# Kernel optimization log

Hardware: AMD Instinct MI355X
Metric: run time of the kernel (lower is better)

## Reference

```python
import jax, jax.numpy as jnp
import numpy as np

B, IN_LEN, N_VARS, PRED_LEN, E, TOPK = 64, 1024, 512, 1024, 8, 2


def setup_inputs() -> dict:
    key = jax.random.key(0)
    k1, k2, k3, k4 = jax.random.split(key, 4)
    x = jax.random.normal(k1, (B, IN_LEN, N_VARS), dtype=jnp.float32)
    # Gating: nn.Linear(seq_len, n_experts, bias=False) -> store as [seq, E] (x @ gate_W)
    gate_W = jax.random.normal(k2, (IN_LEN, E), dtype=jnp.float32) / np.sqrt(IN_LEN).astype(np.float32)
    # experts: nn.Linear(seq_len, pred_len) each -> stacked [E, seq, pred], bias [E, pred]
    expert_W = jax.random.normal(k3, (E, IN_LEN, PRED_LEN), dtype=jnp.float32) / np.sqrt(IN_LEN).astype(np.float32)
    expert_b = jax.random.normal(k4, (E, PRED_LEN), dtype=jnp.float32) * 0.01
    return {"x": x, "gate_W": gate_W, "expert_W": expert_W, "expert_b": expert_b}


def reference(x, gate_W, expert_W, expert_b):
    # x: [B, in_len, n_vars] -> tokens are (batch, variable) pairs of length in_len
    xt = jnp.transpose(x, (0, 2, 1))                      # [B, N, S]
    gate = jax.nn.softmax(xt @ gate_W, axis=-1)           # [B, N, E] (softmaxed logits, as in torch code)
    weights, sel = jax.lax.top_k(gate, TOPK)              # [B, N, K]
    # combine[b,n,e] = sum_k weights[b,n,k] * 1[sel[b,n,k]==e]  (scatter of top-k weights)
    combine = jnp.sum(weights[..., None] * jax.nn.one_hot(sel, E, dtype=x.dtype), axis=2)  # [B, N, E]
    # masked dense combine: identical math to gather->Linear->weighted scatter-add
    out = jnp.zeros((xt.shape[0], xt.shape[1], PRED_LEN), dtype=x.dtype)
    for e in range(E):  # small fixed expert loop
        y_e = xt @ expert_W[e] + expert_b[e]              # [B, N, P]
        out = out + combine[:, :, e:e + 1] * y_e
    out = jnp.transpose(out, (0, 2, 1))                   # [B, pred_len, n_vars]
    gate_mean = jnp.mean(gate, axis=0)                    # [N, E] == gate_logits.mean(dim=0)
    return (out, gate_mean)
```

## Files before the change

kernel.cpp:

```cpp
#include <hip/hip_runtime.h>
#include <cstddef>

typedef __bf16 bf16x8 __attribute__((ext_vector_type(8)));
typedef float  f32x4  __attribute__((ext_vector_type(4)));
typedef unsigned short u16x8 __attribute__((ext_vector_type(8)));

#define GLOBAL_AS __attribute__((address_space(1)))
#define LDS_AS    __attribute__((address_space(3)))

__device__ __forceinline__ void gload_lds16(const void* g, void* l) {
    __builtin_amdgcn_global_load_lds((const GLOBAL_AS unsigned int*)g,
                                     (LDS_AS unsigned int*)l, 16, 0, 0);
}

__device__ __forceinline__ unsigned short f2bf(float f) {
    union { float f; unsigned int u; } v; v.f = f;
    unsigned int r = v.u + 0x7FFFu + ((v.u >> 16) & 1u);
    return (unsigned short)(r >> 16);
}
__device__ __forceinline__ float bf2f(unsigned short h) {
    union { unsigned int u; float f; } v; v.u = ((unsigned int)h) << 16;
    return v.f;
}

__global__ __launch_bounds__(256) void transpose_cast_kernel(
    const float* __restrict__ src, unsigned short* __restrict__ dst,
    int R, int C)
{
    const int bat = blockIdx.z;
    src += (size_t)bat * R * C;
    dst += (size_t)bat * R * C;
    const int r0 = blockIdx.y * 64, c0 = blockIdx.x * 64;
    __shared__ float t[64][65];
    const int tid = threadIdx.x;
    const int rr = tid >> 4;
    const int cc = (tid & 15) * 4;

    #pragma unroll
    for (int p = 0; p < 4; p++) {
        int r = p * 16 + rr;
        const float4 v = *reinterpret_cast<const float4*>(&src[(size_t)(r0 + r) * C + c0 + cc]);
        t[r][cc + 0] = v.x; t[r][cc + 1] = v.y; t[r][cc + 2] = v.z; t[r][cc + 3] = v.w;
    }
    __syncthreads();
    #pragma unroll
    for (int p = 0; p < 4; p++) {
        int c = p * 16 + rr;
        ushort4 o;
        o.x = f2bf(t[cc + 0][c]); o.y = f2bf(t[cc + 1][c]);
        o.z = f2bf(t[cc + 2][c]); o.w = f2bf(t[cc + 3][c]);
        *reinterpret_cast<ushort4*>(&dst[(size_t)(c0 + c) * R + r0 + cc]) = o;
    }
}

__global__ __launch_bounds__(256) void transpose_x_gate_kernel(
    const float* __restrict__ src, const float* __restrict__ gW,
    unsigned short* __restrict__ dst, float* __restrict__ plog)
{
    const int bat = blockIdx.z;
    const int R = 1024, C = 512;
    const float* srcb = src + (size_t)bat * R * C;
    unsigned short* dstb = dst + (size_t)bat * R * C;
    const int r0 = blockIdx.y * 64, c0 = blockIdx.x * 64;
    __shared__ float t[64][65];
    __shared__ float gWs[64][8];
    __shared__ float pacc[4][64][9];
    const int tid = threadIdx.x;
    const int rr = tid >> 4;
    const int cc = (tid & 15) * 4;

    if (tid < 128) {
        reinterpret_cast<float4*>(&gWs[0][0])[tid] =
            reinterpret_cast<const float4*>(gW + (size_t)r0 * 8)[tid];
    }
    #pragma unroll
    for (int p = 0; p < 4; p++) {
        int r = p * 16 + rr;
        const float4 v = *reinterpret_cast<const float4*>(&srcb[(size_t)(r0 + r) * C + c0 + cc]);
        t[r][cc + 0] = v.x; t[r][cc + 1] = v.y; t[r][cc + 2] = v.z; t[r][cc + 3] = v.w;
    }
    __syncthreads();
    #pragma unroll
    for (int p = 0; p < 4; p++) {
        int c = p * 16 + rr;
        ushort4 o;
        o.x = f2bf(t[cc + 0][c]); o.y = f2bf(t[cc + 1][c]);
        o.z = f2bf(t[cc + 2][c]); o.w = f2bf(t[cc + 3][c]);
        *reinterpret_cast<ushort4*>(&dstb[(size_t)(c0 + c) * R + r0 + cc]) = o;
    }

    {
        const int nl = tid & 63;
        const int sc = tid >> 6;
        float a[8];
        #pragma unroll
        for (int e = 0; e < 8; e++) a[e] = 0.f;
        for (int s = sc * 16; s < sc * 16 + 16; s++) {
            float xv = t[s][nl];
            #pragma unroll
            for (int e = 0; e < 8; e++) a[e] = fmaf(xv, gWs[s][e], a[e]);
        }
        #pragma unroll
        for (int e = 0; e < 8; e++) pacc[sc][nl][e] = a[e];
        __syncthreads();
        if (tid < 64) {
            const size_t base = (((size_t)bat * 16 + blockIdx.y) * 512 + c0 + tid) * 8;
            #pragma unroll
            for (int e = 0; e < 8; e++) {
                float v = ((pacc[0][tid][e] + pacc[1][tid][e]) + pacc[2][tid][e]) + pacc[3][tid][e];
                plog[base + e] = v;
            }
        }
    }
}

__global__ __launch_bounds__(256) void gate_stage2_kernel(
    const float* __restrict__ plog,
    float* __restrict__ gate, int* __restrict__ e01,
    float* __restrict__ w0a, float* __restrict__ w1a,
    int* __restrict__ hist)
{
    __shared__ int h[16];
    const int tid = threadIdx.x;
    if (tid < 16) h[tid] = 0;
    __syncthreads();

    const int t = blockIdx.x * 256 + tid;
    const int b = t >> 9;
    const int n = t & 511;

    float acc[8];
    #pragma unroll
    for (int e = 0; e < 8; e++) acc[e] = 0.f;
    for (int y = 0; y < 16; y++) {
        const float* pp = plog + (((size_t)b * 16 + y) * 512 + n) * 8;
        const float4 lo = *reinterpret_cast<const float4*>(pp);
        const float4 hi = *reinterpret_cast<const float4*>(pp + 4);
        acc[0] += lo.x; acc[1] += lo.y; acc[2] += lo.z; acc[3] += lo.w;
        acc[4] += hi.x; acc[5] += hi.y; acc[6] += hi.z; acc[7] += hi.w;
    }
    float m = acc[0];
    #pragma unroll
    for (int e = 1; e < 8; e++) m = fmaxf(m, acc[e]);
    float p[8], s = 0.f;
    #pragma unroll
    for (int e = 0; e < 8; e++) { p[e] = __expf(acc[e] - m); s += p[e]; }
    float inv = 1.f / s;
    #pragma unroll
    for (int e = 0; e < 8; e++) p[e] *= inv;

    int e0 = 0;
    #pragma unroll
    for (int e = 1; e < 8; e++) if (p[e] > p[e0]) e0 = e;
    int e1 = -1;
    #pragma unroll
    for (int e = 0; e < 8; e++) {
        if (e == e0) continue;
        if (e1 < 0 || p[e] > p[e1]) e1 = e;
    }

    const size_t base = (size_t)t * 8;
    #pragma unroll
    for (int e = 0; e < 8; e++) gate[base + e] = p[e];
    e01[t] = e0 | (e1 << 8);
    w0a[t] = p[e0];
    w1a[t] = p[e1];

    atomicAdd(&h[e0], 1);
    atomicAdd(&h[8 + e1], 1);
    __syncthreads();
    if (tid < 16) hist[blockIdx.x * 16 + tid] = h[tid];
}

__global__ __launch_bounds__(256) void gate_mean_kernel(
    const float* __restrict__ gate, float* __restrict__ out)
{
    const int idx = blockIdx.x * 256 + threadIdx.x;
    float s = 0.f;
    #pragma unroll 8
    for (int b = 0; b < 64; b++) s += gate[(size_t)b * 4096 + idx];
    out[idx] = s * (1.f / 64.f);
}

__global__ __launch_bounds__(256) void scan_kernel(
    const int* __restrict__ hist, int* __restrict__ chunk_off,
    int* __restrict__ meta)
{
    __shared__ int cnt_s[16];
    const int tid = threadIdx.x;
    if (tid < 16) {
        int run = 0;
        for (int c = 0; c < 128; c++) {
            chunk_off[c * 16 + tid] = run;
            run += hist[c * 16 + tid];
        }
        cnt_s[tid] = run;
        meta[16 + tid] = run;
    }
    __syncthreads();
    __shared__ int base_s[16];
    if (tid == 0) {
        int run = 0, trun = 0;
        meta[32] = 0;
        for (int g = 0; g < 16; g++) {
            base_s[g] = run;
            meta[g] = run;
            run += cnt_s[g];
            trun += (cnt_s[g] + 255) >> 8;
            meta[33 + g] = trun;
        }
    }
    __syncthreads();
    for (int i = tid; i < 2048; i += 256)
        chunk_off[i] += base_s[i & 15];
}

__global__ __launch_bounds__(256) void fill_kernel(
    const int* __restrict__ e01, const int* __restrict__ chunk_off,
    int* __restrict__ perm, int* __restrict__ posA, int* __restrict__ posB)
{
    __shared__ int wh[4][16];
    const int tid = threadIdx.x;
    const int wv = tid >> 6, lane = tid & 63;
    const int chunk = blockIdx.x;
    const int t = chunk * 256 + tid;
    const int ev = e01[t];
    const int e0 = ev & 255, e1 = ev >> 8;

    const unsigned long long ltmask = (lane == 63) ? 0x7FFFFFFFFFFFFFFFull
                                                   : ((1ull << lane) - 1ull);
    unsigned long long m0sel = 0, m1sel = 0;
    #pragma unroll
    for (int e = 0; e < 8; e++) {
        unsigned long long b0 = __ballot(e0 == e);
        unsigned long long b1 = __ballot(e1 == e);
        if (e0 == e) m0sel = b0;
        if (e1 == e) m1sel = b1;
        if (lane == 0) {
            wh[wv][e]     = __popcll(b0);
            wh[wv][8 + e] = __popcll(b1);
        }
    }
    const int r0l = __popcll(m0sel & ltmask);
    const int r1l = __popcll(m1sel & ltmask);
    __syncthreads();

    int off0 = 0, off1 = 0;
    for (int w = 0; w < wv; w++) { off0 += wh[w][e0]; off1 += wh[w][8 + e1]; }

    const int p0 = chunk_off[chunk * 16 + e0] + off0 + r0l;
    const int p1 = chunk_off[chunk * 16 + 8 + e1] + off1 + r1l;
    perm[p0] = t; perm[p1] = t;
    posA[t] = p0; posB[t] = p1;
}

__global__ __launch_bounds__(512, 2) void grouped_gemm_kernel(
    const unsigned short* __restrict__ Wt,
    const unsigned short* __restrict__ xt,
    const int* __restrict__ perm,
    const int* __restrict__ meta,
    const float* __restrict__ expert_b,
    unsigned short* __restrict__ tmp)
{
    const int d    = blockIdx.x;
    const int xcd  = d & 7;
    const int jj   = d >> 3;
    const int tile = xcd * 34 + (jj >> 2);
    const int p0   = (jj & 3) * 256;

    int g = -1;
    #pragma unroll
    for (int gg = 0; gg < 16; gg++) {
        if (tile >= meta[32 + gg] && tile < meta[33 + gg]) g = gg;
    }
    if (g < 0) return;
    const int lt = tile - meta[32 + g];
    const int e = g & 7;
    const int cnt_local = meta[16 + g] - lt * 256;
    const int pbase = meta[g] + lt * 256;

    __shared__ unsigned short As[2][256 * 64];
    __shared__ unsigned short Bs[2][256 * 64];

    const int tid  = threadIdx.x;
    const int wid  = tid >> 6, lane = tid & 63;
    const int wr = wid >> 2, wc = wid & 3;
    const int q = lane >> 4, r16 = lane & 15;

    const int srow   = tid >> 3;
    const int schunk = tid & 7;
    const int gcol   = (schunk ^ (srow & 7)) * 8;

    const unsigned short* Abase = Wt + (size_t)e * 1024 * 1024;

    int tok[4];
    #pragma unroll
    for (int c = 0; c < 4; c++) {
        int row = c * 64 + srow;
        int idx = row < cnt_local ? row : 0;
        tok[c] = perm[pbase + idx];
    }

    f32x4 acc[8][4];
    #pragma unroll
    for (int m = 0; m < 8; m++)
        #pragma unroll
        for (int nn = 0; nn < 4; nn++)
            acc[m][nn] = (f32x4){0.f, 0.f, 0.f, 0.f};

    #define STAGE(buf, kt) do {                                                   \
        _Pragma("unroll")                                                         \
        for (int c = 0; c < 4; c++) {                                             \
            int row = c * 64 + srow;                                              \
            gload_lds16(Abase + (size_t)(p0 + row) * 1024 + (kt) * 64 + gcol,     \
                        &As[buf][row * 64 + schunk * 8]);                         \
        }                                                                         \
        _Pragma("unroll")                                                         \
        for (int c = 0; c < 4; c++) {                                             \
            int row = c * 64 + srow;                                              \
            gload_lds16(xt + (size_t)tok[c] * 1024 + (kt) * 64 + gcol,            \
                        &Bs[buf][row * 64 + schunk * 8]);                         \
        }                                                                         \
    } while (0)

    const int rsw = r16 & 7;

    STAGE(0, 0);
    STAGE(1, 1);
    asm volatile("s_waitcnt vmcnt(8)" ::: "memory");
    __builtin_amdgcn_sched_barrier(0);
    __builtin_amdgcn_s_barrier();

    #pragma unroll 2
    for (int kt = 0; kt < 16; kt++) {
        const int cur = kt & 1;
        #pragma unroll
        for (int kk = 0; kk < 2; kk++) {
            const int ch = ((kk * 4 + q) ^ rsw) * 8;
            bf16x8 af[8], bfr[4];
            #pragma unroll
            for (int m = 0; m < 8; m++)
                af[m] = *reinterpret_cast<const bf16x8*>(
                    &As[cur][(wr * 128 + m * 16 + r16) * 64 + ch]);
            #pragma unroll
            for (int nn = 0; nn < 4; nn++)
                bfr[nn] = *reinterpret_cast<const bf16x8*>(
                    &Bs[cur][(wc * 64 + nn * 16 + r16) * 64 + ch]);
            #pragma unroll
            for (int m = 0; m < 8; m++)
                #pragma unroll
                for (int nn = 0; nn < 4; nn++)
                    acc[m][nn] = __builtin_amdgcn_mfma_f32_16x16x32_bf16(
                        af[m], bfr[nn], acc[m][nn], 0, 0, 0);
        }
        __builtin_amdgcn_sched_barrier(0);
        __builtin_amdgcn_s_barrier();
        if (kt < 14) {
            STAGE(cur, kt + 2);
            asm volatile("s_waitcnt vmcnt(8)" ::: "memory");
        } else {
            asm volatile("s_waitcnt vmcnt(0)" ::: "memory");
        }
        __builtin_amdgcn_sched_barrier(0);
        __builtin_amdgcn_s_barrier();
    }
    #undef STAGE

    float bv[8][4];
    #pragma unroll
    for (int m = 0; m < 8; m++)
        #pragma unroll
        for (int r = 0; r < 4; r++)
            bv[m][r] = expert_b[e * 1024 + p0 + wr * 128 + m * 16 + q * 4 + r];

    #pragma unroll
    for (int nn = 0; nn < 4; nn++) {
        const int j = wc * 64 + nn * 16 + r16;
        if (j < cnt_local) {
            const size_t rowb = (size_t)(pbase + j) * 1024;
            #pragma unroll
            for (int m = 0; m < 8; m++) {
                ushort4 o;
                o.x = f2bf(acc[m][nn][0] + bv[m][0]);
                o.y = f2bf(acc[m][nn][1] + bv[m][1]);
                o.z = f2bf(acc[m][nn][2] + bv[m][2]);
                o.w = f2bf(acc[m][nn][3] + bv[m][3]);
                *reinterpret_cast<ushort4*>(&tmp[rowb + p0 + wr * 128 + m * 16 + q * 4]) = o;
            }
        }
    }
}

__global__ __launch_bounds__(256) void combine_kernel(
    const unsigned short* __restrict__ tmp,
    const int* __restrict__ posA, const int* __restrict__ posB,
    const float* __restrict__ w0a, const float* __restrict__ w1a,
    float* __restrict__ out)
{
    __shared__ unsigned short l0[64 * 128];
    __shared__ unsigned short l1[64 * 128];
    __shared__ float sw0[64], sw1[64];
    const int tid = threadIdx.x;
    const int b = blockIdx.z;
    const int p0 = blockIdx.y * 128;
    const int n0 = blockIdx.x * 64;

    if (tid < 64) {
        int t = b * 512 + n0 + tid;
        sw0[tid] = w0a[t];
        sw1[tid] = w1a[t];
    }

    #pragma unroll
    for (int pass = 0; pass < 8; pass++) {
        int rowid = pass * 16 + (tid >> 4);
        int slot = rowid >> 6, j = rowid & 63;
        int t = b * 512 + n0 + j;
        int pos = slot ? posB[t] : posA[t];
        u16x8 v = *reinterpret_cast<const u16x8*>(&tmp[(size_t)pos * 1024 + p0 + (tid & 15) * 8]);
        unsigned short* dst = slot ? l1 : l0;
        int c0 = (tid & 15) * 8;
        int sw = (j & 31) << 2;
        ushort4 a; a.x = v[0]; a.y = v[1]; a.z = v[2]; a.w = v[3];
        ushort4 bq; bq.x = v[4]; bq.y = v[5]; bq.z = v[6]; bq.w = v[7];
        *reinterpret_cast<ushort4*>(&dst[j * 128 + (c0 ^ sw)]) = a;
        *reinterpret_cast<ushort4*>(&dst[j * 128 + ((c0 + 4) ^ sw)]) = bq;
    }
    __syncthreads();

    const int j = tid & 63;
    const int wv = tid >> 6;
    const float wa = sw0[j], wb = sw1[j];
    const int sw = (j & 31) << 2;
    #pragma unroll 8
    for (int pp = 0; pp < 32; pp++) {
        int p = wv * 32 + pp;
        float v0 = bf2f(l0[j * 128 + (p ^ sw)]);
        float v1 = bf2f(l1[j * 128 + (p ^ sw)]);
        out[((size_t)b * 1024 + p0 + p) * 512 + n0 + j] = wa * v0 + wb * v1;
    }
}

__global__ __launch_bounds__(256, 2) void moe_dense_idx_kernel(
    const unsigned short* __restrict__ Wt,
    const unsigned short* __restrict__ xt,
    const int* __restrict__ e01,
    const float* __restrict__ w0a, const float* __restrict__ w1a,
    const float* __restrict__ expert_b,
    float* __restrict__ out)
{
    __shared__ unsigned short As[128 * 64];
    __shared__ unsigned short Bs[128 * 64];

    const int tid  = threadIdx.x;
    const int wave = tid >> 6, lane = tid & 63;
    const int wr = wave >> 1, wc = wave & 1;
    const int q = lane >> 4, r16 = lane & 15;
    const int b  = blockIdx.z;
    const int p0 = blockIdx.y * 128;
    const int n0 = blockIdx.x * 128;

    const unsigned short* Bbase = xt + (size_t)b * 512 * 1024;
    const int srow = tid >> 3;
    const int scol = (tid & 7) * 8;

    f32x4 out_acc[4][4];
    #pragma unroll
    for (int m = 0; m < 4; m++)
        #pragma unroll
        for (int nn = 0; nn < 4; nn++)
            out_acc[m][nn] = (f32x4){0.f, 0.f, 0.f, 0.f};

    for (int e = 0; e < 8; e++) {
        const unsigned short* Abase = Wt + (size_t)e * 1024 * 1024;
        f32x4 acc[4][4];
        #pragma unroll
        for (int m = 0; m < 4; m++)
            #pragma unroll
            for (int nn = 0; nn < 4; nn++)
                acc[m][nn] = (f32x4){0.f, 0.f, 0.f, 0.f};

        for (int kt = 0; kt < 16; kt++) {
            __syncthreads();
            #pragma unroll
            for (int c = 0; c < 4; c++) {
                int row = c * 32 + srow;
                gload_lds16(Abase + (size_t)(p0 + row) * 1024 + kt * 64 + scol,
                            &As[row * 64 + scol]);
            }
            #pragma unroll
            for (int c = 0; c < 4; c++) {
                int row = c * 32 + srow;
                gload_lds16(Bbase + (size_t)(n0 + row) * 1024 + kt * 64 + scol,
                            &Bs[row * 64 + scol]);
            }
            __syncthreads();
            #pragma unroll
            for (int kk = 0; kk < 2; kk++) {
                bf16x8 af[4], bfr[4];
                #pragma unroll
                for (int m = 0; m < 4; m++) {
                    af[m]  = *reinterpret_cast<const bf16x8*>(&As[(wr * 64 + m * 16 + r16) * 64 + kk * 32 + q * 8]);
                    bfr[m] = *reinterpret_cast<const bf16x8*>(&Bs[(wc * 64 + m * 16 + r16) * 64 + kk * 32 + q * 8]);
                }
                #pragma unroll
                for (int m = 0; m < 4; m++)
                    #pragma unroll
                    for (int nn = 0; nn < 4; nn++)
                        acc[m][nn] = __builtin_amdgcn_mfma_f32_16x16x32_bf16(
                            af[m], bfr[nn], acc[m][nn], 0, 0, 0);
            }
        }
        float cw[4], bv[4][4];
        #pragma unroll
        for (int nn = 0; nn < 4; nn++) {
            int t = b * 512 + n0 + wc * 64 + nn * 16 + r16;
            int ev = e01[t];
            cw[nn] = (e == (ev & 255)) ? w0a[t] : ((e == (ev >> 8)) ? w1a[t] : 0.f);
        }
        #pragma unroll
        for (int m = 0; m < 4; m++)
            #pragma unroll
            for (int r = 0; r < 4; r++)
                bv[m][r] = expert_b[e * 1024 + p0 + wr * 64 + m * 16 + q * 4 + r];
        #pragma unroll
        for (int m = 0; m < 4; m++)
            #pragma unroll
            for (int nn = 0; nn < 4; nn++)
                #pragma unroll
                for (int r = 0; r < 4; r++)
                    out_acc[m][nn][r] += cw[nn] * (acc[m][nn][r] + bv[m][r]);
    }
    #pragma unroll
    for (int m = 0; m < 4; m++)
        #pragma unroll
        for (int nn = 0; nn < 4; nn++)
            #pragma unroll
            for (int r = 0; r < 4; r++) {
                int p = p0 + wr * 64 + m * 16 + q * 4 + r;
                int n = n0 + wc * 64 + nn * 16 + r16;
                out[(size_t)b * 1024 * 512 + (size_t)p * 512 + n] = out_acc[m][nn][r];
            }
}

extern "C" void kernel_launch(void* const* d_in, const int* in_sizes, int n_in,
                              void* d_out, int out_size, void* d_ws, size_t ws_size,
                              hipStream_t stream) {
    const float* x        = (const float*)d_in[0];
    const float* gate_W   = (const float*)d_in[1];
    const float* expert_W = (const float*)d_in[2];
    const float* expert_b = (const float*)d_in[3];
    float* out = (float*)d_out;

    char* ws = (char*)d_ws;
    unsigned short* Wt  = (unsigned short*)(ws + 0);
    unsigned short* xt  = (unsigned short*)(ws + 16777216);
    float* gate  = (float*)(ws + 83886080);
    float* w0a   = (float*)(ws + 84934656);
    float* w1a   = (float*)(ws + 85065728);
    int*   e01   = (int*)(ws + 85196800);
    int*   hist  = (int*)(ws + 85327872);
    int*   coff  = (int*)(ws + 85336064);
    int*   meta  = (int*)(ws + 85344256);
    int*   perm  = (int*)(ws + 85344512);
    int*   posA  = (int*)(ws + 85606656);
    int*   posB  = (int*)(ws + 85737728);
    unsigned short* tmp = (unsigned short*)(ws + 85868800);
    float* plog = (float*)(ws + 85868800);
    const size_t NEEDED = 85868800ull + 134217728ull;

    transpose_cast_kernel<<<dim3(16, 16, 8), 256, 0, stream>>>(expert_W, Wt, 1024, 1024);
    transpose_x_gate_kernel<<<dim3(8, 16, 64), 256, 0, stream>>>(x, gate_W, xt, plog);

    gate_stage2_kernel<<<128, 256, 0, stream>>>(plog, gate, e01, w0a, w1a, hist);
    gate_mean_kernel<<<16, 256, 0, stream>>>(gate, out + 33554432);

    if (ws_size >= NEEDED) {
        scan_kernel<<<1, 256, 0, stream>>>(hist, coff, meta);
        fill_kernel<<<128, 256, 0, stream>>>(e01, coff, perm, posA, posB);
        grouped_gemm_kernel<<<dim3(1088), 512, 0, stream>>>(Wt, xt, perm, meta, expert_b, tmp);
        combine_kernel<<<dim3(8, 8, 64), 256, 0, stream>>>(tmp, posA, posB, w0a, w1a, out);
    } else {
        moe_dense_idx_kernel<<<dim3(4, 8, 64), 256, 0, stream>>>(Wt, xt, e01, w0a, w1a, expert_b, out);
    }
}
```

Before: 315.6 us.

## Split GEMM main loop into quadrant phases with interleaved prefetch and setprio

```diff
diff --git a/kernel.cpp b/kernel.cpp
--- a/kernel.cpp
+++ b/kernel.cpp
@@ -286,17 +286,18 @@
     const int wid  = tid >> 6, lane = tid & 63;
     const int wr = wid >> 2, wc = wid & 3;
     const int q = lane >> 4, r16 = lane & 15;
-
-    const int srow   = tid >> 3;
+    const int rsw = r16 & 7;
+
+    const int srow8  = tid >> 3;
     const int schunk = tid & 7;
-    const int gcol   = (schunk ^ (srow & 7)) * 8;
+    const int gcol   = (schunk ^ (srow8 & 7)) * 8;
 
     const unsigned short* Abase = Wt + (size_t)e * 1024 * 1024;
 
     int tok[4];
     #pragma unroll
     for (int c = 0; c < 4; c++) {
-        int row = c * 64 + srow;
+        int row = c * 64 + srow8;
         int idx = row < cnt_local ? row : 0;
         tok[c] = perm[pbase + idx];
     }
@@ -308,63 +309,111 @@
         for (int nn = 0; nn < 4; nn++)
             acc[m][nn] = (f32x4){0.f, 0.f, 0.f, 0.f};
 
-    #define STAGE(buf, kt) do {                                                   \
-        _Pragma("unroll")                                                         \
-        for (int c = 0; c < 4; c++) {                                             \
-            int row = c * 64 + srow;                                              \
-            gload_lds16(Abase + (size_t)(p0 + row) * 1024 + (kt) * 64 + gcol,     \
-                        &As[buf][row * 64 + schunk * 8]);                         \
-        }                                                                         \
-        _Pragma("unroll")                                                         \
-        for (int c = 0; c < 4; c++) {                                             \
-            int row = c * 64 + srow;                                              \
-            gload_lds16(xt + (size_t)tok[c] * 1024 + (kt) * 64 + gcol,            \
-                        &Bs[buf][row * 64 + schunk * 8]);                         \
-        }                                                                         \
-    } while (0)
-
-    const int rsw = r16 & 7;
-
-    STAGE(0, 0);
-    STAGE(1, 1);
-    asm volatile("s_waitcnt vmcnt(8)" ::: "memory");
-    __builtin_amdgcn_sched_barrier(0);
-    __builtin_amdgcn_s_barrier();
+    bf16x8 afr[8];
+    bf16x8 bfr[2][4];
+
+    #define STAGE_A(buf, kt, half) do {                                          \
+        _Pragma("unroll")                                                        \
+        for (int r = 0; r < 2; r++) {                                            \
+            int row = (half) * 128 + r * 64 + srow8;                             \
+            gload_lds16(Abase + (size_t)(p0 + row) * 1024 + (kt) * 64 + gcol,    \
+                        &As[buf][row * 64 + schunk * 8]);                        \
+        } } while (0)
+    #define STAGE_B(buf, kt, half) do {                                          \
+        _Pragma("unroll")                                                        \
+        for (int r = 0; r < 2; r++) {                                            \
+            int row = (half) * 128 + r * 64 + srow8;                             \
+            gload_lds16(xt + (size_t)tok[(half) * 2 + r] * 1024 + (kt) * 64 + gcol, \
+                        &Bs[buf][row * 64 + schunk * 8]);                        \
+        } } while (0)
+
+    #define DS_A(MH) do {                                                        \
+        _Pragma("unroll")                                                        \
+        for (int m = 0; m < 4; m++)                                              \
+            _Pragma("unroll")                                                    \
+            for (int kk = 0; kk < 2; kk++)                                       \
+                afr[m * 2 + kk] = *reinterpret_cast<const bf16x8*>(              \
+                    &As[cur][(wr * 128 + (MH) * 64 + m * 16 + r16) * 64          \
+                             + (((kk * 4 + q) ^ rsw) * 8)]);                     \
+        } while (0)
+    #define DS_B(NH) do {                                                        \
+        _Pragma("unroll")                                                        \
+        for (int nn = 0; nn < 2; nn++)                                           \
+            _Pragma("unroll")                                                    \
+            for (int kk = 0; kk < 2; kk++)                                       \
+                bfr[NH][nn * 2 + kk] = *reinterpret_cast<const bf16x8*>(         \
+                    &Bs[cur][(wc * 64 + (NH) * 32 + nn * 16 + r16) * 64          \
+                             + (((kk * 4 + q) ^ rsw) * 8)]);                     \
+        } while (0)
+
+    #define MFMA_Q(MH, NH) do {                                                  \
+        __builtin_amdgcn_s_setprio(1);                                           \
+        _Pragma("unroll")                                                        \
+        for (int kk = 0; kk < 2; kk++)                                           \
+            _Pragma("unroll")                                                    \
+            for (int m = 0; m < 4; m++)                                          \
+                _Pragma("unroll")                                                \
+                for (int nn = 0; nn < 2; nn++)                                   \
+                    acc[(MH) * 4 + m][(NH) * 2 + nn] =                           \
+                        __builtin_amdgcn_mfma_f32_16x16x32_bf16(                 \
+                            afr[m * 2 + kk], bfr[NH][nn * 2 + kk],               \
+                            acc[(MH) * 4 + m][(NH) * 2 + nn], 0, 0, 0);          \
+        __builtin_amdgcn_s_setprio(0);                                           \
+        } while (0)
+
+    #define SBAR do {                                                            \
+        __builtin_amdgcn_sched_barrier(0);                                       \
+        __builtin_amdgcn_s_barrier();                                            \
+        __builtin_amdgcn_sched_barrier(0);                                       \
+        } while (0)
+
+    STAGE_A(0, 0, 0); STAGE_A(0, 0, 1);
+    STAGE_B(0, 0, 0); STAGE_B(0, 0, 1);
+    STAGE_B(1, 1, 0); STAGE_B(1, 1, 1);
+    asm volatile("s_waitcnt vmcnt(4)" ::: "memory");
+    SBAR;
 
     #pragma unroll 2
     for (int kt = 0; kt < 16; kt++) {
         const int cur = kt & 1;
-        #pragma unroll
-        for (int kk = 0; kk < 2; kk++) {
-            const int ch = ((kk * 4 + q) ^ rsw) * 8;
-            bf16x8 af[8], bfr[4];
-            #pragma unroll
-            for (int m = 0; m < 8; m++)
-                af[m] = *reinterpret_cast<const bf16x8*>(
-                    &As[cur][(wr * 128 + m * 16 + r16) * 64 + ch]);
-            #pragma unroll
-            for (int nn = 0; nn < 4; nn++)
-                bfr[nn] = *reinterpret_cast<const bf16x8*>(
-                    &Bs[cur][(wc * 64 + nn * 16 + r16) * 64 + ch]);
-            #pragma unroll
-            for (int m = 0; m < 8; m++)
-                #pragma unroll
-                for (int nn = 0; nn < 4; nn++)
-                    acc[m][nn] = __builtin_amdgcn_mfma_f32_16x16x32_bf16(
-                        af[m], bfr[nn], acc[m][nn], 0, 0, 0);
-        }
-        __builtin_amdgcn_sched_barrier(0);
-        __builtin_amdgcn_s_barrier();
-        if (kt < 14) {
-            STAGE(cur, kt + 2);
-            asm volatile("s_waitcnt vmcnt(8)" ::: "memory");
-        } else {
+        const int nxt = cur ^ 1;
+
+        DS_A(0); DS_B(0);
+        if (kt < 15) STAGE_A(nxt, kt + 1, 0);
+        asm volatile("s_waitcnt lgkmcnt(8)" ::: "memory");
+        SBAR;
+        MFMA_Q(0, 0);
+        SBAR;
+
+        DS_B(1);
+        if (kt < 15) STAGE_A(nxt, kt + 1, 1);
+        SBAR;
+        MFMA_Q(0, 1);
+        SBAR;
+
+        DS_A(1);
+        if (kt < 14) STAGE_B(cur, kt + 2, 0);
+        SBAR;
+        MFMA_Q(1, 0);
+        SBAR;
+
+        if (kt < 14) STAGE_B(cur, kt + 2, 1);
+        SBAR;
+        MFMA_Q(1, 1);
+        if (kt <= 13) {
+            asm volatile("s_waitcnt vmcnt(4)" ::: "memory");
+        } else if (kt == 14) {
             asm volatile("s_waitcnt vmcnt(0)" ::: "memory");
         }
-        __builtin_amdgcn_sched_barrier(0);
-        __builtin_amdgcn_s_barrier();
-    }
-    #undef STAGE
+        SBAR;
+    }
+
+    #undef STAGE_A
+    #undef STAGE_B
+    #undef DS_A
+    #undef DS_B
+    #undef MFMA_Q
+    #undef SBAR
 
     float bv[8][4];
     #pragma unroll
```

Result: faster. 306.5 us (-2.9%).
